# Kernel tuning notes

Measured on AMD Instinct MI355X. Metric: run time of the kernel, lower is better.

Reference implementation:

```python
import jax, jax.numpy as jnp
import numpy as np

B, L, HIDDEN, HEAD_DIM = 8, 1024, 1024, 64


def setup_inputs() -> dict:
    key = jax.random.key(0)
    ks = jax.random.split(key, 11)
    s = 1.0 / np.sqrt(HIDDEN)
    return {
        "query": jax.random.normal(ks[0], (B, L, HIDDEN), jnp.float32),
        "key": jax.random.normal(ks[1], (B, L, HIDDEN), jnp.float32),
        "value": jax.random.normal(ks[2], (B, L, HIDDEN), jnp.float32),
        "k_bias_matrix": jax.random.normal(ks[3], (L, L, HEAD_DIM), jnp.float32) * 0.02,
        "v_bias_matrix": jax.random.normal(ks[4], (L, L, HEAD_DIM), jnp.float32) * 0.02,
        "Wq": jax.random.normal(ks[5], (HIDDEN, HEAD_DIM), jnp.float32) * s,
        "bq": jnp.zeros((HEAD_DIM,), jnp.float32),
        "Wk": jax.random.normal(ks[6], (HIDDEN, HEAD_DIM), jnp.float32) * s,
        "bk": jnp.zeros((HEAD_DIM,), jnp.float32),
        "Wv": jax.random.normal(ks[7], (HIDDEN, HEAD_DIM), jnp.float32) * s,
        "bv": jnp.zeros((HEAD_DIM,), jnp.float32),
        "mask": jnp.ones((B, L), jnp.int32),
    }


def reference(query, key, value, k_bias_matrix, v_bias_matrix, Wq, bq, Wk, bk, Wv, bv, mask):
    # projections to head_dim
    q = query @ Wq + bq  # [B,L,D]
    k = key @ Wk + bk    # [B,L,D]
    v = value @ Wv + bv  # [B,L,D]
    # content scores + relative key-bias scores (Shaw et al.)
    attn_1 = jnp.einsum('bqd,bkd->bqk', q, k)              # [B,L,L]
    attn_2 = jnp.einsum('bqd,qkd->bqk', q, k_bias_matrix)  # [B,L,L]
    scores = (attn_1 + attn_2) / jnp.sqrt(jnp.asarray(q.shape[-1], q.dtype))
    scores = jnp.where(mask[:, None, :] == 0, jnp.asarray(-1e9, scores.dtype), scores)
    w = jax.nn.softmax(scores, axis=-1)                    # [B,L,L]
    values_1 = jnp.einsum('bqk,bkd->bqd', w, v)
    values_2 = jnp.einsum('bqk,qkd->bqd', w, v_bias_matrix)
    return values_1 + values_2
```

## Files before the change

### kernel.cpp

```cpp
#include <hip/hip_runtime.h>

#define B_ 8
#define L_ 1024
#define HID_ 1024
#define D_ 64

typedef short bf16x8 __attribute__((ext_vector_type(8)));
typedef float f32x4 __attribute__((ext_vector_type(4)));

__device__ inline short f2bf(float f) {
    unsigned u = __builtin_bit_cast(unsigned, f);
    unsigned r = (u + 0x7fffu + ((u >> 16) & 1u)) >> 16;
    return (short)r;
}

__global__ __launch_bounds__(256) void proj_kernel(
    const float* __restrict__ query, const float* __restrict__ key, const float* __restrict__ value,
    const float* __restrict__ Wq, const float* __restrict__ bq,
    const float* __restrict__ Wk, const float* __restrict__ bk,
    const float* __restrict__ Wv, const float* __restrict__ bv,
    float* __restrict__ qp, float* __restrict__ kp, float* __restrict__ vp)
{
    const int which = blockIdx.y;
    const float* in   = which == 0 ? query : (which == 1 ? key : value);
    const float* W    = which == 0 ? Wq : (which == 1 ? Wk : Wv);
    const float* bias = which == 0 ? bq : (which == 1 ? bk : bv);
    float* out        = which == 0 ? qp : (which == 1 ? kp : vp);

    __shared__ float Xs[64][68];
    __shared__ float Ws[64][64];

    const int t  = threadIdx.x;
    const int tx = t & 15;
    const int ty = t >> 4;
    const int r0 = blockIdx.x * 64;

    float acc[4][4] = {};
    for (int kk = 0; kk < HID_; kk += 64) {
        {
            const int r  = t >> 4;
            const int c4 = t & 15;
            #pragma unroll
            for (int i = 0; i < 4; i++) {
                float4 x = *(const float4*)(in + (size_t)(r0 + r + 16 * i) * HID_ + kk + 4 * c4);
                *(float4*)(&Xs[r + 16 * i][4 * c4]) = x;
                float4 w = *(const float4*)(W + (size_t)(kk + r + 16 * i) * D_ + 4 * c4);
                *(float4*)(&Ws[r + 16 * i][4 * c4]) = w;
            }
        }
        __syncthreads();
        #pragma unroll 8
        for (int k = 0; k < 64; k++) {
            float4 b4 = *(const float4*)(&Ws[k][4 * tx]);
            #pragma unroll
            for (int i = 0; i < 4; i++) {
                float a = Xs[4 * ty + i][k];
                acc[i][0] += a * b4.x;
                acc[i][1] += a * b4.y;
                acc[i][2] += a * b4.z;
                acc[i][3] += a * b4.w;
            }
        }
        __syncthreads();
    }
    float4 bb = *(const float4*)(bias + 4 * tx);
    #pragma unroll
    for (int i = 0; i < 4; i++) {
        float4 o;
        o.x = acc[i][0] + bb.x; o.y = acc[i][1] + bb.y;
        o.z = acc[i][2] + bb.z; o.w = acc[i][3] + bb.w;
        *(float4*)(out + (size_t)(r0 + 4 * ty + i) * D_ + 4 * tx) = o;
    }
}

__global__ __launch_bounds__(256) void attn1_kernel(
    const float* __restrict__ qp, const float* __restrict__ kp,
    const int* __restrict__ mask, float* __restrict__ s1)
{
    const int b  = blockIdx.z;
    const int q0 = blockIdx.y * 128;
    const int k0 = blockIdx.x * 128;
    __shared__ float qs[128][68];
    __shared__ float ks[128][68];
    const int t = threadIdx.x;
    {
        const int row = t >> 4;
        const int c4  = t & 15;
        #pragma unroll
        for (int i = 0; i < 8; i++) {
            int r = row + 16 * i;
            *(float4*)&qs[r][c4 * 4] = *(const float4*)(qp + ((size_t)b * L_ + q0 + r) * D_ + c4 * 4);
            *(float4*)&ks[r][c4 * 4] = *(const float4*)(kp + ((size_t)b * L_ + k0 + r) * D_ + c4 * 4);
        }
    }
    __syncthreads();
    const int tx = t & 15, ty = t >> 4;
    float acc[8][8] = {};
    for (int d4 = 0; d4 < 16; d4++) {
        float4 qv[8], kv[8];
        #pragma unroll
        for (int i = 0; i < 8; i++) qv[i] = *(const float4*)&qs[ty + 16 * i][d4 * 4];
        #pragma unroll
        for (int j = 0; j < 8; j++) kv[j] = *(const float4*)&ks[tx + 16 * j][d4 * 4];
        #pragma unroll
        for (int i = 0; i < 8; i++)
            #pragma unroll
            for (int j = 0; j < 8; j++)
                acc[i][j] += qv[i].x * kv[j].x + qv[i].y * kv[j].y +
                             qv[i].z * kv[j].z + qv[i].w * kv[j].w;
    }
    #pragma unroll
    for (int j = 0; j < 8; j++) {
        int kg = k0 + tx + 16 * j;
        bool live = mask[b * L_ + kg] != 0;
        #pragma unroll
        for (int i = 0; i < 8; i++) {
            int qg = q0 + ty + 16 * i;
            s1[((size_t)b * L_ + qg) * L_ + kg] = live ? acc[i][j] * 0.125f : -1e9f;
        }
    }
}

#define KS_ 1032
__global__ __launch_bounds__(512) void row_kernel(
    const float* __restrict__ qp, const float* __restrict__ kb,
    const float* __restrict__ vb, float* __restrict__ s1w,
    float* __restrict__ out)
{
    __shared__ float sc[2 * 8 * KS_];
    __shared__ short qbf[2 * 16 * 64];
    const int t = threadIdx.x;
    const int wave = t >> 6, lane = t & 63;
    const int q0 = blockIdx.x * 2;

    #pragma unroll
    for (int i = 0; i < 4; i++) {
        int idx = t + 512 * i;
        int d = idx & 63, bq = idx >> 6;
        int b = bq & 15, q = bq >> 4;
        float v = (b < 8) ? 0.125f * qp[((size_t)b * L_ + q0 + q) * D_ + d] : 0.0f;
        qbf[idx] = f2bf(v);
    }
    __syncthreads();

    for (int job = wave; job < 128; job += 8) {
        int q = job >> 6, kt = job & 63;
        int k0 = kt * 16;
        const float* abase = kb + ((size_t)(q0 + q) * L_ + k0 + (lane & 15)) * D_ + (lane >> 4) * 8;
        f32x4 acc = {0.f, 0.f, 0.f, 0.f};
        #pragma unroll
        for (int h = 0; h < 2; h++) {
            float4 x0 = *(const float4*)(abase + h * 32);
            float4 x1 = *(const float4*)(abase + h * 32 + 4);
            bf16x8 a;
            a[0] = f2bf(x0.x); a[1] = f2bf(x0.y); a[2] = f2bf(x0.z); a[3] = f2bf(x0.w);
            a[4] = f2bf(x1.x); a[5] = f2bf(x1.y); a[6] = f2bf(x1.z); a[7] = f2bf(x1.w);
            bf16x8 bq = *(const bf16x8*)&qbf[(q * 16 + (lane & 15)) * 64 + h * 32 + (lane >> 4) * 8];
            acc = __builtin_amdgcn_mfma_f32_16x16x32_bf16(a, bq, acc, 0, 0, 0);
        }
        int b = lane & 15;
        if (b < 8) {
            float* dst = &sc[(q * 8 + b) * KS_ + k0 + (lane >> 4) * 4];
            dst[0] = acc[0]; dst[1] = acc[1]; dst[2] = acc[2]; dst[3] = acc[3];
        }
    }
    __syncthreads();

    #pragma unroll
    for (int i = 0; i < 8; i++) {
        int idx = t + 512 * i;
        int c4 = idx & 255;
        int row = idx >> 8;
        int b = row & 7, q = row >> 3;
        float4 s = *(const float4*)(s1w + ((size_t)b * L_ + q0 + q) * L_ + c4 * 4);
        float* dst = &sc[(q * 8 + b) * KS_ + c4 * 4];
        float4 cur = *(float4*)dst;
        cur.x += s.x; cur.y += s.y; cur.z += s.z; cur.w += s.w;
        *(float4*)dst = cur;
    }
    __syncthreads();

    for (int r = wave; r < 16; r += 8) {
        int q = r >> 3, b = r & 7;
        float* rowp = &sc[r * KS_];
        float* wrow = s1w + ((size_t)b * L_ + q0 + q) * L_;
        float4 x[4];
        float m = -1e30f;
        #pragma unroll
        for (int j = 0; j < 4; j++) {
            x[j] = *(const float4*)&rowp[lane * 4 + 256 * j];
            m = fmaxf(m, fmaxf(fmaxf(x[j].x, x[j].y), fmaxf(x[j].z, x[j].w)));
        }
        #pragma unroll
        for (int off = 32; off; off >>= 1) m = fmaxf(m, __shfl_xor(m, off));
        float s = 0.f;
        #pragma unroll
        for (int j = 0; j < 4; j++) {
            x[j].x = __expf(x[j].x - m); x[j].y = __expf(x[j].y - m);
            x[j].z = __expf(x[j].z - m); x[j].w = __expf(x[j].w - m);
            s += x[j].x + x[j].y + x[j].z + x[j].w;
        }
        #pragma unroll
        for (int off = 32; off; off >>= 1) s += __shfl_xor(s, off);
        float inv = 1.0f / s;
        #pragma unroll
        for (int j = 0; j < 4; j++) {
            x[j].x *= inv; x[j].y *= inv; x[j].z *= inv; x[j].w *= inv;
            *(float4*)&rowp[lane * 4 + 256 * j] = x[j];
            *(float4*)&wrow[lane * 4 + 256 * j] = x[j];
        }
    }
    __syncthreads();

    {
        const int q  = wave >> 2;
        const int kqi = wave & 3;
        const int kq = kqi * 256;
        const int kl = lane >> 4;
        const int d4 = lane & 15;
        float acc[8][4] = {};
        const float* vbbase = vb + ((size_t)(q0 + q) * L_ + kq + kl) * D_ + d4 * 4;
        #pragma unroll 4
        for (int j = 0; j < 64; j++) {
            int k = kq + j * 4 + kl;
            float4 vb4 = *(const float4*)(vbbase + (size_t)j * 4 * D_);
            #pragma unroll
            for (int b = 0; b < 8; b++) {
                float wgt = sc[(q * 8 + b) * KS_ + k];
                acc[b][0] += wgt * vb4.x;
                acc[b][1] += wgt * vb4.y;
                acc[b][2] += wgt * vb4.z;
                acc[b][3] += wgt * vb4.w;
            }
        }
        #pragma unroll
        for (int b = 0; b < 8; b++)
            #pragma unroll
            for (int j = 0; j < 4; j++) {
                float v = acc[b][j];
                v += __shfl_down(v, 32);
                v += __shfl_down(v, 16);
                acc[b][j] = v;
            }
        __syncthreads();
        float* part = sc;
        if (lane < 16) {
            #pragma unroll
            for (int b = 0; b < 8; b++) {
                float4 o; o.x = acc[b][0]; o.y = acc[b][1]; o.z = acc[b][2]; o.w = acc[b][3];
                *(float4*)&part[(((q * 4 + kqi) * 8) + b) * 64 + d4 * 4] = o;
            }
        }
        __syncthreads();
        for (int i = t; i < 1024; i += 512) {
            int d = i & 63; int bq = i >> 6; int b = bq & 7; int q2 = bq >> 3;
            float s = part[((q2 * 4 + 0) * 8 + b) * 64 + d] +
                      part[((q2 * 4 + 1) * 8 + b) * 64 + d] +
                      part[((q2 * 4 + 2) * 8 + b) * 64 + d] +
                      part[((q2 * 4 + 3) * 8 + b) * 64 + d];
            out[((size_t)b * L_ + q0 + q2) * D_ + d] = s;
        }
    }
}

__global__ __launch_bounds__(256) void pv_kernel(
    const float* __restrict__ w, const float* __restrict__ vp, float* __restrict__ out)
{
    const int b  = blockIdx.y;
    const int q0 = blockIdx.x * 32;
    __shared__ float ws_[32][68];
    __shared__ float vs[64][64];
    const int t  = threadIdx.x;
    const int tx = t & 15;
    const int ty = t >> 4;
    float acc[2][4] = {};
    for (int kk = 0; kk < L_; kk += 64) {
        #pragma unroll
        for (int i = 0; i < 2; i++) {
            int f4 = t + 256 * i;
            int qi = f4 >> 4, kc = f4 & 15;
            float4 x = *(const float4*)(w + ((size_t)b * L_ + q0 + qi) * L_ + kk + 4 * kc);
            *(float4*)(&ws_[qi][4 * kc]) = x;
        }
        #pragma unroll
        for (int i = 0; i < 4; i++) {
            int f4 = t + 256 * i;
            int kr = f4 >> 4, dc = f4 & 15;
            float4 x = *(const float4*)(vp + ((size_t)b * L_ + kk + kr) * D_ + 4 * dc);
            *(float4*)(&vs[kr][4 * dc]) = x;
        }
        __syncthreads();
        #pragma unroll 8
        for (int k = 0; k < 64; k++) {
            float4 v4 = *(const float4*)(&vs[k][4 * tx]);
            float a0 = ws_[2 * ty][k], a1 = ws_[2 * ty + 1][k];
            acc[0][0] += a0 * v4.x; acc[0][1] += a0 * v4.y;
            acc[0][2] += a0 * v4.z; acc[0][3] += a0 * v4.w;
            acc[1][0] += a1 * v4.x; acc[1][1] += a1 * v4.y;
            acc[1][2] += a1 * v4.z; acc[1][3] += a1 * v4.w;
        }
        __syncthreads();
    }
    #pragma unroll
    for (int i = 0; i < 2; i++) {
        float* dst = out + ((size_t)b * L_ + q0 + 2 * ty + i) * D_ + 4 * tx;
        float4 o = *(const float4*)dst;
        o.x += acc[i][0]; o.y += acc[i][1]; o.z += acc[i][2]; o.w += acc[i][3];
        *(float4*)dst = o;
    }
}

extern "C" void kernel_launch(void* const* d_in, const int* in_sizes, int n_in,
                              void* d_out, int out_size, void* d_ws, size_t ws_size,
                              hipStream_t stream)
{
    const float* query = (const float*)d_in[0];
    const float* key   = (const float*)d_in[1];
    const float* value = (const float*)d_in[2];
    const float* kb    = (const float*)d_in[3];
    const float* vb    = (const float*)d_in[4];
    const float* Wq    = (const float*)d_in[5];
    const float* bq    = (const float*)d_in[6];
    const float* Wk    = (const float*)d_in[7];
    const float* bk    = (const float*)d_in[8];
    const float* Wv    = (const float*)d_in[9];
    const float* bv    = (const float*)d_in[10];
    const int*   mask  = (const int*)d_in[11];
    float* out = (float*)d_out;

    float* ws = (float*)d_ws;
    const size_t PROJ = (size_t)B_ * L_ * D_;
    float* qp = ws;
    float* kp = ws + PROJ;
    float* vp = ws + 2 * PROJ;
    float* s1 = ws + 3 * PROJ;

    proj_kernel<<<dim3(128, 3), 256, 0, stream>>>(query, key, value,
                                                  Wq, bq, Wk, bk, Wv, bv,
                                                  qp, kp, vp);
    attn1_kernel<<<dim3(8, 8, 8), 256, 0, stream>>>(qp, kp, mask, s1);
    row_kernel<<<512, 512, 0, stream>>>(qp, kb, vb, s1, out);
    pv_kernel<<<dim3(32, 8), 256, 0, stream>>>(s1, vp, out);
}
```

Measured before the change: 691.9 us.

## Fuse content scores, softmax and PV into one kernel with split-bf16 MFMA

Removes the separate attn1 and pv kernels along with the B×L×L fp32 score buffer. Content scores q·k are now computed inside the row kernel on MFMA, with q and k stored as hi/lo bf16 pairs to keep precision, and the mask is applied in the softmax. The v-projection contribution is accumulated in the same loop as the v_bias term. This avoids writing and re-reading about 32MB of scores, at the cost of more MFMA work per block (q·k is recomputed for every key for each block's two query rows) and heavier register pressure.

```diff
diff --git a/kernel.cpp b/kernel.cpp
--- a/kernel.cpp
+++ b/kernel.cpp
@@ -4,6 +4,7 @@
 #define L_ 1024
 #define HID_ 1024
 #define D_ 64
+#define KS_ 1032
 
 typedef short bf16x8 __attribute__((ext_vector_type(8)));
 typedef float f32x4 __attribute__((ext_vector_type(4)));
@@ -12,6 +13,10 @@
     unsigned u = __builtin_bit_cast(unsigned, f);
     unsigned r = (u + 0x7fffu + ((u >> 16) & 1u)) >> 16;
     return (short)r;
+}
+__device__ inline float bf2f(short h) {
+    unsigned u = ((unsigned)(unsigned short)h) << 16;
+    return __builtin_bit_cast(float, u);
 }
 
 __global__ __launch_bounds__(256) void proj_kernel(
@@ -19,13 +24,14 @@
     const float* __restrict__ Wq, const float* __restrict__ bq,
     const float* __restrict__ Wk, const float* __restrict__ bk,
     const float* __restrict__ Wv, const float* __restrict__ bv,
-    float* __restrict__ qp, float* __restrict__ kp, float* __restrict__ vp)
+    unsigned short* __restrict__ qhi, unsigned short* __restrict__ qlo,
+    unsigned short* __restrict__ khi, unsigned short* __restrict__ klo,
+    float* __restrict__ vp)
 {
     const int which = blockIdx.y;
     const float* in   = which == 0 ? query : (which == 1 ? key : value);
     const float* W    = which == 0 ? Wq : (which == 1 ? Wk : Wv);
     const float* bias = which == 0 ? bq : (which == 1 ? bk : bv);
-    float* out        = which == 0 ? qp : (which == 1 ? kp : vp);
 
     __shared__ float Xs[64][68];
     __shared__ float Ws[64][64];
@@ -64,89 +70,66 @@
         __syncthreads();
     }
     float4 bb = *(const float4*)(bias + 4 * tx);
-    #pragma unroll
-    for (int i = 0; i < 4; i++) {
-        float4 o;
-        o.x = acc[i][0] + bb.x; o.y = acc[i][1] + bb.y;
-        o.z = acc[i][2] + bb.z; o.w = acc[i][3] + bb.w;
-        *(float4*)(out + (size_t)(r0 + 4 * ty + i) * D_ + 4 * tx) = o;
-    }
-}
-
-__global__ __launch_bounds__(256) void attn1_kernel(
-    const float* __restrict__ qp, const float* __restrict__ kp,
-    const int* __restrict__ mask, float* __restrict__ s1)
-{
-    const int b  = blockIdx.z;
-    const int q0 = blockIdx.y * 128;
-    const int k0 = blockIdx.x * 128;
-    __shared__ float qs[128][68];
-    __shared__ float ks[128][68];
-    const int t = threadIdx.x;
-    {
-        const int row = t >> 4;
-        const int c4  = t & 15;
-        #pragma unroll
-        for (int i = 0; i < 8; i++) {
-            int r = row + 16 * i;
-            *(float4*)&qs[r][c4 * 4] = *(const float4*)(qp + ((size_t)b * L_ + q0 + r) * D_ + c4 * 4);
-            *(float4*)&ks[r][c4 * 4] = *(const float4*)(kp + ((size_t)b * L_ + k0 + r) * D_ + c4 * 4);
-        }
-    }
-    __syncthreads();
-    const int tx = t & 15, ty = t >> 4;
-    float acc[8][8] = {};
-    for (int d4 = 0; d4 < 16; d4++) {
-        float4 qv[8], kv[8];
-        #pragma unroll
-        for (int i = 0; i < 8; i++) qv[i] = *(const float4*)&qs[ty + 16 * i][d4 * 4];
-        #pragma unroll
-        for (int j = 0; j < 8; j++) kv[j] = *(const float4*)&ks[tx + 16 * j][d4 * 4];
-        #pragma unroll
-        for (int i = 0; i < 8; i++)
-            #pragma unroll
-            for (int j = 0; j < 8; j++)
-                acc[i][j] += qv[i].x * kv[j].x + qv[i].y * kv[j].y +
-                             qv[i].z * kv[j].z + qv[i].w * kv[j].w;
-    }
-    #pragma unroll
-    for (int j = 0; j < 8; j++) {
-        int kg = k0 + tx + 16 * j;
-        bool live = mask[b * L_ + kg] != 0;
-        #pragma unroll
-        for (int i = 0; i < 8; i++) {
-            int qg = q0 + ty + 16 * i;
-            s1[((size_t)b * L_ + qg) * L_ + kg] = live ? acc[i][j] * 0.125f : -1e9f;
-        }
-    }
-}
-
-#define KS_ 1032
-__global__ __launch_bounds__(512) void row_kernel(
-    const float* __restrict__ qp, const float* __restrict__ kb,
-    const float* __restrict__ vb, float* __restrict__ s1w,
-    float* __restrict__ out)
+    if (which == 2) {
+        #pragma unroll
+        for (int i = 0; i < 4; i++) {
+            float4 o;
+            o.x = acc[i][0] + bb.x; o.y = acc[i][1] + bb.y;
+            o.z = acc[i][2] + bb.z; o.w = acc[i][3] + bb.w;
+            *(float4*)(vp + (size_t)(r0 + 4 * ty + i) * D_ + 4 * tx) = o;
+        }
+    } else {
+        const float sgain = (which == 0) ? 0.125f : 1.0f;
+        unsigned short* hid = (which == 0) ? qhi : khi;
+        unsigned short* lod = (which == 0) ? qlo : klo;
+        #pragma unroll
+        for (int i = 0; i < 4; i++) {
+            float v0 = sgain * (acc[i][0] + bb.x);
+            float v1 = sgain * (acc[i][1] + bb.y);
+            float v2 = sgain * (acc[i][2] + bb.z);
+            float v3 = sgain * (acc[i][3] + bb.w);
+            short h0 = f2bf(v0), h1 = f2bf(v1), h2 = f2bf(v2), h3 = f2bf(v3);
+            ushort4 hv, lv;
+            hv.x = (unsigned short)h0; hv.y = (unsigned short)h1;
+            hv.z = (unsigned short)h2; hv.w = (unsigned short)h3;
+            lv.x = (unsigned short)f2bf(v0 - bf2f(h0));
+            lv.y = (unsigned short)f2bf(v1 - bf2f(h1));
+            lv.z = (unsigned short)f2bf(v2 - bf2f(h2));
+            lv.w = (unsigned short)f2bf(v3 - bf2f(h3));
+            size_t off = (size_t)(r0 + 4 * ty + i) * D_ + 4 * tx;
+            *(ushort4*)(hid + off) = hv;
+            *(ushort4*)(lod + off) = lv;
+        }
+    }
+}
+
+__global__ __launch_bounds__(512, 4) void mega_kernel(
+    const float* __restrict__ kb, const float* __restrict__ vb,
+    const float* __restrict__ vp,
+    const unsigned short* __restrict__ qhi, const unsigned short* __restrict__ qlo,
+    const unsigned short* __restrict__ khi, const unsigned short* __restrict__ klo,
+    const int* __restrict__ mask, float* __restrict__ out)
 {
     __shared__ float sc[2 * 8 * KS_];
-    __shared__ short qbf[2 * 16 * 64];
+    __shared__ unsigned short qb2[2 * 16 * D_];
     const int t = threadIdx.x;
     const int wave = t >> 6, lane = t & 63;
+    const int lr = lane & 15, lg = lane >> 4;
     const int q0 = blockIdx.x * 2;
 
-    #pragma unroll
-    for (int i = 0; i < 4; i++) {
-        int idx = t + 512 * i;
-        int d = idx & 63, bq = idx >> 6;
-        int b = bq & 15, q = bq >> 4;
-        float v = (b < 8) ? 0.125f * qp[((size_t)b * L_ + q0 + q) * D_ + d] : 0.0f;
-        qbf[idx] = f2bf(v);
+    {
+        int d4 = t & 15, row = (t >> 4) & 15, q = t >> 8;
+        int b = row >> 1;
+        const unsigned short* src = (row & 1) ? qlo : qhi;
+        ushort4 v = *(const ushort4*)(src + ((size_t)b * L_ + q0 + q) * D_ + 4 * d4);
+        *(ushort4*)&qb2[(q * 16 + row) * D_ + 4 * d4] = v;
     }
     __syncthreads();
 
-    for (int job = wave; job < 128; job += 8) {
-        int q = job >> 6, kt = job & 63;
-        int k0 = kt * 16;
-        const float* abase = kb + ((size_t)(q0 + q) * L_ + k0 + (lane & 15)) * D_ + (lane >> 4) * 8;
+    for (int jj = 0; jj < 16; jj++) {
+        int job = wave + jj * 8;
+        int q = job >> 6, k0 = (job & 63) * 16;
+        const float* abase = kb + ((size_t)(q0 + q) * L_ + k0 + lr) * D_ + lg * 8;
         f32x4 acc = {0.f, 0.f, 0.f, 0.f};
         #pragma unroll
         for (int h = 0; h < 2; h++) {
@@ -155,49 +138,91 @@
             bf16x8 a;
             a[0] = f2bf(x0.x); a[1] = f2bf(x0.y); a[2] = f2bf(x0.z); a[3] = f2bf(x0.w);
             a[4] = f2bf(x1.x); a[5] = f2bf(x1.y); a[6] = f2bf(x1.z); a[7] = f2bf(x1.w);
-            bf16x8 bq = *(const bf16x8*)&qbf[(q * 16 + (lane & 15)) * 64 + h * 32 + (lane >> 4) * 8];
-            acc = __builtin_amdgcn_mfma_f32_16x16x32_bf16(a, bq, acc, 0, 0, 0);
-        }
-        int b = lane & 15;
-        if (b < 8) {
-            float* dst = &sc[(q * 8 + b) * KS_ + k0 + (lane >> 4) * 4];
-            dst[0] = acc[0]; dst[1] = acc[1]; dst[2] = acc[2]; dst[3] = acc[3];
+            bf16x8 qf = *(const bf16x8*)&qb2[(q * 16 + lr) * D_ + h * 32 + lg * 8];
+            acc = __builtin_amdgcn_mfma_f32_16x16x32_bf16(a, qf, acc, 0, 0, 0);
+        }
+        float s0 = acc[0] + __shfl_xor(acc[0], 1);
+        float s1 = acc[1] + __shfl_xor(acc[1], 1);
+        float s2 = acc[2] + __shfl_xor(acc[2], 1);
+        float s3 = acc[3] + __shfl_xor(acc[3], 1);
+        if (!(lane & 1)) {
+            int b = lr >> 1;
+            float* dst = &sc[(q * 8 + b) * KS_ + k0 + lg * 4];
+            dst[0] = s0; dst[1] = s1; dst[2] = s2; dst[3] = s3;
         }
     }
     __syncthreads();
 
+    {
+        bf16x8 qf[2][2];
+        #pragma unroll
+        for (int q = 0; q < 2; q++)
+            #pragma unroll
+            for (int s = 0; s < 2; s++)
+                qf[q][s] = *(const bf16x8*)&qb2[(q * 16 + lr) * D_ + s * 32 + lg * 8];
+
+        int job = wave;
+        size_t off0 = ((size_t)((job >> 6) & 7) * L_ + (job & 63) * 16 + lr) * D_ + lg * 8;
+        bf16x8 nh0 = *(const bf16x8*)(khi + off0);
+        bf16x8 nh1 = *(const bf16x8*)(khi + off0 + 32);
+        bf16x8 nl0 = *(const bf16x8*)(klo + off0);
+        bf16x8 nl1 = *(const bf16x8*)(klo + off0 + 32);
+        for (int jj = 0; jj < 128; jj++) {
+            int q = job >> 9, b = (job >> 6) & 7, k0 = (job & 63) * 16;
+            bf16x8 ah0 = nh0, ah1 = nh1, al0 = nl0, al1 = nl1;
+            int nj = job + 8;
+            if (jj < 127) {
+                size_t noff = ((size_t)((nj >> 6) & 7) * L_ + (nj & 63) * 16 + lr) * D_ + lg * 8;
+                nh0 = *(const bf16x8*)(khi + noff);
+                nh1 = *(const bf16x8*)(khi + noff + 32);
+                nl0 = *(const bf16x8*)(klo + noff);
+                nl1 = *(const bf16x8*)(klo + noff + 32);
+            }
+            f32x4 acc = {0.f, 0.f, 0.f, 0.f};
+            acc = __builtin_amdgcn_mfma_f32_16x16x32_bf16(ah0, qf[q][0], acc, 0, 0, 0);
+            acc = __builtin_amdgcn_mfma_f32_16x16x32_bf16(al0, qf[q][0], acc, 0, 0, 0);
+            acc = __builtin_amdgcn_mfma_f32_16x16x32_bf16(ah1, qf[q][1], acc, 0, 0, 0);
+            acc = __builtin_amdgcn_mfma_f32_16x16x32_bf16(al1, qf[q][1], acc, 0, 0, 0);
+            float s0 = acc[0] + __shfl_xor(acc[0], 1);
+            float s1 = acc[1] + __shfl_xor(acc[1], 1);
+            float s2 = acc[2] + __shfl_xor(acc[2], 1);
+            float s3 = acc[3] + __shfl_xor(acc[3], 1);
+            if (lr == 2 * b) {
+                float4* dst = (float4*)&sc[(q * 8 + b) * KS_ + k0 + lg * 4];
+                float4 cur = *dst;
+                cur.x += s0; cur.y += s1; cur.z += s2; cur.w += s3;
+                *dst = cur;
+            }
+            job = nj;
+        }
+    }
+    __syncthreads();
+
     #pragma unroll
-    for (int i = 0; i < 8; i++) {
-        int idx = t + 512 * i;
-        int c4 = idx & 255;
-        int row = idx >> 8;
-        int b = row & 7, q = row >> 3;
-        float4 s = *(const float4*)(s1w + ((size_t)b * L_ + q0 + q) * L_ + c4 * 4);
-        float* dst = &sc[(q * 8 + b) * KS_ + c4 * 4];
-        float4 cur = *(float4*)dst;
-        cur.x += s.x; cur.y += s.y; cur.z += s.z; cur.w += s.w;
-        *(float4*)dst = cur;
-    }
-    __syncthreads();
-
-    for (int r = wave; r < 16; r += 8) {
-        int q = r >> 3, b = r & 7;
+    for (int rr = 0; rr < 2; rr++) {
+        int r = wave + rr * 8;
+        int b = r & 7;
         float* rowp = &sc[r * KS_];
-        float* wrow = s1w + ((size_t)b * L_ + q0 + q) * L_;
+        const int* mrow = mask + b * L_;
         float4 x[4];
-        float m = -1e30f;
+        float mx = -1e30f;
         #pragma unroll
         for (int j = 0; j < 4; j++) {
             x[j] = *(const float4*)&rowp[lane * 4 + 256 * j];
-            m = fmaxf(m, fmaxf(fmaxf(x[j].x, x[j].y), fmaxf(x[j].z, x[j].w)));
-        }
-        #pragma unroll
-        for (int off = 32; off; off >>= 1) m = fmaxf(m, __shfl_xor(m, off));
+            int4 mm = *(const int4*)&mrow[lane * 4 + 256 * j];
+            x[j].x = mm.x ? x[j].x : -1e9f;
+            x[j].y = mm.y ? x[j].y : -1e9f;
+            x[j].z = mm.z ? x[j].z : -1e9f;
+            x[j].w = mm.w ? x[j].w : -1e9f;
+            mx = fmaxf(mx, fmaxf(fmaxf(x[j].x, x[j].y), fmaxf(x[j].z, x[j].w)));
+        }
+        #pragma unroll
+        for (int off = 32; off; off >>= 1) mx = fmaxf(mx, __shfl_xor(mx, off));
         float s = 0.f;
         #pragma unroll
         for (int j = 0; j < 4; j++) {
-            x[j].x = __expf(x[j].x - m); x[j].y = __expf(x[j].y - m);
-            x[j].z = __expf(x[j].z - m); x[j].w = __expf(x[j].w - m);
+            x[j].x = __expf(x[j].x - mx); x[j].y = __expf(x[j].y - mx);
+            x[j].z = __expf(x[j].z - mx); x[j].w = __expf(x[j].w - mx);
             s += x[j].x + x[j].y + x[j].z + x[j].w;
         }
         #pragma unroll
@@ -207,30 +232,33 @@
         for (int j = 0; j < 4; j++) {
             x[j].x *= inv; x[j].y *= inv; x[j].z *= inv; x[j].w *= inv;
             *(float4*)&rowp[lane * 4 + 256 * j] = x[j];
-            *(float4*)&wrow[lane * 4 + 256 * j] = x[j];
         }
     }
     __syncthreads();
 
     {
-        const int q  = wave >> 2;
+        const int q   = wave >> 2;
         const int kqi = wave & 3;
-        const int kq = kqi * 256;
-        const int kl = lane >> 4;
-        const int d4 = lane & 15;
+        const int kq  = kqi * 256;
+        const int kl  = lane >> 4;
+        const int d4  = lane & 15;
         float acc[8][4] = {};
         const float* vbbase = vb + ((size_t)(q0 + q) * L_ + kq + kl) * D_ + d4 * 4;
-        #pragma unroll 4
+        const float* vpbase = vp + ((size_t)(kq + kl)) * D_ + d4 * 4;
         for (int j = 0; j < 64; j++) {
+            float4 vb4 = *(const float4*)(vbbase + (size_t)j * 4 * D_);
+            float4 vp4[8];
+            #pragma unroll
+            for (int b = 0; b < 8; b++)
+                vp4[b] = *(const float4*)(vpbase + (size_t)b * L_ * D_ + (size_t)j * 4 * D_);
             int k = kq + j * 4 + kl;
-            float4 vb4 = *(const float4*)(vbbase + (size_t)j * 4 * D_);
             #pragma unroll
             for (int b = 0; b < 8; b++) {
                 float wgt = sc[(q * 8 + b) * KS_ + k];
-                acc[b][0] += wgt * vb4.x;
-                acc[b][1] += wgt * vb4.y;
-                acc[b][2] += wgt * vb4.z;
-                acc[b][3] += wgt * vb4.w;
+                acc[b][0] += wgt * vb4.x;    acc[b][1] += wgt * vb4.y;
+                acc[b][2] += wgt * vb4.z;    acc[b][3] += wgt * vb4.w;
+                acc[b][0] += wgt * vp4[b].x; acc[b][1] += wgt * vp4[b].y;
+                acc[b][2] += wgt * vp4[b].z; acc[b][3] += wgt * vp4[b].w;
             }
         }
         #pragma unroll
@@ -260,53 +288,6 @@
                       part[((q2 * 4 + 3) * 8 + b) * 64 + d];
             out[((size_t)b * L_ + q0 + q2) * D_ + d] = s;
         }
-    }
-}
-
-__global__ __launch_bounds__(256) void pv_kernel(
-    const float* __restrict__ w, const float* __restrict__ vp, float* __restrict__ out)
-{
-    const int b  = blockIdx.y;
-    const int q0 = blockIdx.x * 32;
-    __shared__ float ws_[32][68];
-    __shared__ float vs[64][64];
-    const int t  = threadIdx.x;
-    const int tx = t & 15;
-    const int ty = t >> 4;
-    float acc[2][4] = {};
-    for (int kk = 0; kk < L_; kk += 64) {
-        #pragma unroll
-        for (int i = 0; i < 2; i++) {
-            int f4 = t + 256 * i;
-            int qi = f4 >> 4, kc = f4 & 15;
-            float4 x = *(const float4*)(w + ((size_t)b * L_ + q0 + qi) * L_ + kk + 4 * kc);
-            *(float4*)(&ws_[qi][4 * kc]) = x;
-        }
-        #pragma unroll
-        for (int i = 0; i < 4; i++) {
-            int f4 = t + 256 * i;
-            int kr = f4 >> 4, dc = f4 & 15;
-            float4 x = *(const float4*)(vp + ((size_t)b * L_ + kk + kr) * D_ + 4 * dc);
-            *(float4*)(&vs[kr][4 * dc]) = x;
-        }
-        __syncthreads();
-        #pragma unroll 8
-        for (int k = 0; k < 64; k++) {
-            float4 v4 = *(const float4*)(&vs[k][4 * tx]);
-            float a0 = ws_[2 * ty][k], a1 = ws_[2 * ty + 1][k];
-            acc[0][0] += a0 * v4.x; acc[0][1] += a0 * v4.y;
-            acc[0][2] += a0 * v4.z; acc[0][3] += a0 * v4.w;
-            acc[1][0] += a1 * v4.x; acc[1][1] += a1 * v4.y;
-            acc[1][2] += a1 * v4.z; acc[1][3] += a1 * v4.w;
-        }
-        __syncthreads();
-    }
-    #pragma unroll
-    for (int i = 0; i < 2; i++) {
-        float* dst = out + ((size_t)b * L_ + q0 + 2 * ty + i) * D_ + 4 * tx;
-        float4 o = *(const float4*)dst;
-        o.x += acc[i][0]; o.y += acc[i][1]; o.z += acc[i][2]; o.w += acc[i][3];
-        *(float4*)dst = o;
     }
 }
 
@@ -328,17 +309,15 @@
     const int*   mask  = (const int*)d_in[11];
     float* out = (float*)d_out;
 
-    float* ws = (float*)d_ws;
     const size_t PROJ = (size_t)B_ * L_ * D_;
-    float* qp = ws;
-    float* kp = ws + PROJ;
-    float* vp = ws + 2 * PROJ;
-    float* s1 = ws + 3 * PROJ;
+    unsigned short* qhi = (unsigned short*)d_ws;
+    unsigned short* qlo = qhi + PROJ;
+    unsigned short* khi = qlo + PROJ;
+    unsigned short* klo = khi + PROJ;
+    float*          vp  = (float*)(klo + PROJ);
 
     proj_kernel<<<dim3(128, 3), 256, 0, stream>>>(query, key, value,
                                                   Wq, bq, Wk, bk, Wv, bv,
-                                                  qp, kp, vp);
-    attn1_kernel<<<dim3(8, 8, 8), 256, 0, stream>>>(qp, kp, mask, s1);
-    row_kernel<<<512, 512, 0, stream>>>(qp, kb, vb, s1, out);
-    pv_kernel<<<dim3(32, 8), 256, 0, stream>>>(s1, vp, out);
-}
+                                                  qhi, qlo, khi, klo, vp);
+    mega_kernel<<<512, 512, 0, stream>>>(kb, vb, vp, qhi, qlo, khi, klo, mask, out);
+}
```

Result: slower. 1.562 ms (+125.8%).
